# Optimization experiments

Hardware: AMD Instinct MI355X
Metric: run time of the kernel (lower is better)

Reference implementation:

```python
import jax, jax.numpy as jnp
import numpy as np

N_NODES = 65536   # 64 graphs * 1024 nodes
N_EDGES = 1048576
B, S = 64, 1024   # graphs, nodes per graph (regular batching)
C_IN, H = 4, 128


def _p(key, shape, scale=0.05):
    return scale * jax.random.normal(key, shape, dtype=jnp.float32)


def setup_inputs() -> dict:
    ks = jax.random.split(jax.random.key(0), 32)
    x = jax.random.normal(ks[0], (N_NODES, C_IN), dtype=jnp.float32)
    # edges drawn uniformly over nodes (PyG [2, E] convention)
    edge_index = jax.random.randint(ks[1], (2, N_EDGES), 0, N_NODES)
    batch = jnp.repeat(jnp.arange(B), S)  # contiguous, equal-size graphs
    inp = {"x": x, "edge_index": edge_index, "batch": batch}
    # GCN layers
    inp["gW1"] = _p(ks[2], (C_IN, H)); inp["gb1"] = jnp.zeros((H,), jnp.float32)
    inp["gW2"] = _p(ks[3], (H, H));    inp["gb2"] = jnp.zeros((H,), jnp.float32)
    # Residual block 1 (C_IN -> H, 1x1 conv shortcut). BN in eval mode with
    # running_mean=0, running_var=1 folds to gamma*x + beta.
    inp["r1w1"] = _p(ks[4], (H, C_IN, 3)); inp["r1b1"] = jnp.zeros((H,), jnp.float32)
    inp["r1g1"] = jnp.ones((H,), jnp.float32); inp["r1be1"] = jnp.zeros((H,), jnp.float32)
    inp["r1w2"] = _p(ks[5], (H, H, 3)); inp["r1b2"] = jnp.zeros((H,), jnp.float32)
    inp["r1g2"] = jnp.ones((H,), jnp.float32); inp["r1be2"] = jnp.zeros((H,), jnp.float32)
    inp["r1sw"] = _p(ks[6], (H, C_IN, 1)); inp["r1sb"] = jnp.zeros((H,), jnp.float32)
    # Residual block 2 (H -> H, identity shortcut)
    inp["r2w1"] = _p(ks[7], (H, H, 3)); inp["r2b1"] = jnp.zeros((H,), jnp.float32)
    inp["r2g1"] = jnp.ones((H,), jnp.float32); inp["r2be1"] = jnp.zeros((H,), jnp.float32)
    inp["r2w2"] = _p(ks[8], (H, H, 3)); inp["r2b2"] = jnp.zeros((H,), jnp.float32)
    inp["r2g2"] = jnp.ones((H,), jnp.float32); inp["r2be2"] = jnp.zeros((H,), jnp.float32)
    return inp


def _gcn(h, W, b, row, col, dinv_row, dinv_col, n):
    # PyG GCNConv: h' = D^-1/2 (A + I) D^-1/2 (h W) + b
    hw = h @ W                                   # [n, out]
    norm = dinv_row * dinv_col                   # [E+n]
    msg = norm[:, None] * hw[row]                # gather src
    return jax.ops.segment_sum(msg, col, num_segments=n) + b


def _conv1d(x, w, b, pad):
    y = jax.lax.conv_general_dilated(x, w, (1,), [(pad, pad)],
                                     dimension_numbers=("NCH", "OIH", "NCH"))
    return y + b[None, :, None]


def _resblock(x, w1, b1, g1, be1, w2, b2, g2, be2, sw=None, sb=None):
    y = _conv1d(x, w1, b1, 1)
    y = jax.nn.relu(g1[None, :, None] * y + be1[None, :, None])
    y = _conv1d(y, w2, b2, 1)
    y = g2[None, :, None] * y + be2[None, :, None]
    sc = x if sw is None else _conv1d(x, sw, sb, 0)
    return jax.nn.relu(y + sc)


def reference(x, edge_index, batch, gW1, gb1, gW2, gb2,
              r1w1, r1b1, r1g1, r1be1, r1w2, r1b2, r1g2, r1be2, r1sw, r1sb,
              r2w1, r2b1, r2g1, r2be1, r2w2, r2b2, r2g2, r2be2):
    n = x.shape[0]
    loop = jnp.arange(n)
    row = jnp.concatenate([edge_index[0], loop])   # src (+ self loops)
    col = jnp.concatenate([edge_index[1], loop])   # dst (+ self loops)
    deg = jax.ops.segment_sum(jnp.ones_like(col, dtype=x.dtype), col, num_segments=n)
    dinv = jnp.where(deg > 0, jax.lax.rsqrt(deg), 0.0)
    dinv_row, dinv_col = dinv[row], dinv[col]

    h = jax.nn.relu(_gcn(x, gW1, gb1, row, col, dinv_row, dinv_col, n))
    h = jax.nn.relu(_gcn(h, gW2, gb2, row, col, dinv_row, dinv_col, n))

    # to_dense_batch: batch is contiguous with S nodes per graph -> reshape,
    # then transpose to [B, C, S] for Conv1d.
    xd = x.reshape(B, S, C_IN).transpose(0, 2, 1)
    f = _resblock(xd, r1w1, r1b1, r1g1, r1be1, r1w2, r1b2, r1g2, r1be2, r1sw, r1sb)
    f = _resblock(f, r2w1, r2b1, r2g1, r2be1, r2w2, r2b2, r2g2, r2be2)
    global_reps = f.mean(axis=2)                   # [B, H]
    return h, global_reps
```

## Files before the change

### kernel.cpp

```cpp
#include <hip/hip_runtime.h>
#include <hip/hip_bf16.h>
#include <cstddef>
#include <cstdint>

#define NN 65536
#define NE 1048576
#define BGR 64
#define SGR 1024
#define HH 128
#define BCAP 5120
#define SSTRIDE 64

typedef unsigned short ushort_t;
typedef __attribute__((ext_vector_type(8))) short short8v;
typedef __attribute__((ext_vector_type(4))) float f32x4;

static __device__ inline ushort_t f2bf(float f) {
    __hip_bfloat16 h = __float2bfloat16(f);
    return *reinterpret_cast<ushort_t*>(&h);
}
static __device__ inline float bflo(unsigned int u) { return __uint_as_float(u << 16); }
static __device__ inline float bfhi(unsigned int u) { return __uint_as_float(u & 0xffff0000u); }


__global__ void prep_k(const float* __restrict__ r1w1, const float* __restrict__ r1w2,
                       const float* __restrict__ r2w1, const float* __restrict__ r2w2,
                       const float* __restrict__ gW2,
                       float* __restrict__ wT1, ushort_t* __restrict__ wbB,
                       ushort_t* __restrict__ wbC, ushort_t* __restrict__ wbD,
                       ushort_t* __restrict__ w2T, ushort_t* __restrict__ zA,
                       ushort_t* __restrict__ f1, float* __restrict__ gout,
                       int* __restrict__ bucketFill) {
    int gid = blockIdx.x * 256 + threadIdx.x;
    if (gid < 1536) {
        int o = gid & 127, k = (gid >> 7) % 3, ci = gid / 384;
        wT1[ci * 384 + k * 128 + o] = r1w1[o * 12 + ci * 3 + k];
    } else if (gid < 1536 + 3 * 49152) {
        int idx = gid - 1536;
        int which = idx / 49152; idx -= which * 49152;
        int ci = idx & 127, o = (idx >> 7) & 127, k = idx >> 14;
        const float* w = which == 0 ? r1w2 : (which == 1 ? r2w1 : r2w2);
        ushort_t* wb = which == 0 ? wbB : (which == 1 ? wbC : wbD);
        wb[idx] = f2bf(w[o * 384 + ci * 3 + k]);
    } else if (gid < 1536 + 3 * 49152 + 16384) {
        int idx = gid - (1536 + 3 * 49152);
        int k = idx & 127, h = idx >> 7;
        w2T[idx] = f2bf(gW2[k * 128 + h]);
    } else if (gid < 1536 + 3 * 49152 + 16384 + 16384) {
        int idx = gid - (1536 + 3 * 49152 + 16384);
        int b = idx >> 8, r = (idx >> 7) & 1, c = idx & 127;
        size_t off = ((size_t)b * 1026 + (r ? 1025 : 0)) * 128 + c;
        zA[off] = 0;
        f1[off] = 0;
    } else if (gid < 1536 + 3 * 49152 + 16384 + 16384 + 8192) {
        gout[gid - (1536 + 3 * 49152 + 16384 + 16384)] = 0.f;
    } else if (gid < 1536 + 3 * 49152 + 16384 + 16384 + 8192 + 256) {
        bucketFill[gid - (1536 + 3 * 49152 + 16384 + 16384 + 8192)] = 0;
    }
}


static __device__ __forceinline__ void binA_body(int blk,
        const int* __restrict__ row, const int* __restrict__ col,
        int* __restrict__ bucketFill, unsigned* __restrict__ region) {
    __shared__ int lcnt[256], lbase[256], lcur[256];
    int t = threadIdx.x;
    lcnt[t] = 0;
    __syncthreads();
    int e0 = blk * 4096;
    int r[16], c[16];
    #pragma unroll
    for (int i = 0; i < 16; ++i) {
        int e = e0 + i * 256 + t;
        r[i] = row[e];
        c[i] = col[e];
        atomicAdd(&lcnt[(unsigned)c[i] >> 8], 1);
    }
    __syncthreads();
    lbase[t] = atomicAdd(&bucketFill[t], lcnt[t]);
    lcur[t] = 0;
    __syncthreads();
    #pragma unroll
    for (int i = 0; i < 16; ++i) {
        int bkt = (unsigned)c[i] >> 8;
        int pos = lbase[bkt] + atomicAdd(&lcur[bkt], 1);
        if (pos < BCAP)
            region[bkt * BCAP + pos] = ((unsigned)r[i] << 8) | ((unsigned)c[i] & 255u);
    }
}

static __device__ __forceinline__ void binB_body(int blk,
        const unsigned* __restrict__ region, const int* __restrict__ bucketFill,
        unsigned* __restrict__ slots4, int* __restrict__ cnts, float* __restrict__ dinv) {
    __shared__ int deg[256], cur[256];
    int t = threadIdx.x, b = blk;
    deg[t] = 0;
    __syncthreads();
    int cnt = min(bucketFill[b], BCAP);
    const unsigned* reg = region + b * BCAP;
    for (int i = t; i < cnt; i += 256)
        atomicAdd(&deg[reg[i] & 255u], 1);
    __syncthreads();
    int dg = deg[t];
    int n = (b << 8) + t;
    cnts[n] = dg;
    dinv[n] = rsqrtf((float)(dg + 1));
    cur[t] = 0;
    __syncthreads();
    for (int i = t; i < cnt; i += 256) {
        unsigned en = reg[i];
        int d8 = en & 255u;
        int rk = atomicAdd(&cur[d8], 1);
        if (rk < 63)
            slots4[((size_t)((b << 8) + d8)) * SSTRIDE + rk] = en >> 8;
    }
    __syncthreads();
    int L = min(dg, 63);
    size_t base = (size_t)n * SSTRIDE;
    slots4[base + L] = (unsigned)n;
    int E8 = (L + 8) & ~7;
    for (int j = L + 1; j < E8; ++j) slots4[base + j] = 0xFFFFFFFFu;
}


static __device__ __forceinline__ void aggx_body(int blk,
        const float* __restrict__ x, const int* __restrict__ cnts,
        const float* __restrict__ dinv, unsigned* __restrict__ slots4,
        const float* __restrict__ W1, const float* __restrict__ b1,
        ushort_t* __restrict__ h1out) {
    int w = threadIdx.x >> 6, lane = threadIdx.x & 63;
    int n = blk * 4 + w;
    int L = min(cnts[n], 63);
    int E8 = (L + 8) & ~7;
    float dn = dinv[n];
    size_t base = (size_t)n * SSTRIDE;
    unsigned src = (unsigned)n;
    float wgt = 0.f;
    if (lane < E8) {
        unsigned e = slots4[base + lane];
        if (e != 0xFFFFFFFFu) { src = e; wgt = dn * dinv[e]; }
        slots4[base + lane] = ((unsigned)f2bf(wgt) << 16) | src;
    }
    float4 xv = *(const float4*)&x[(size_t)src * 4];
    float a0 = wgt * xv.x, a1 = wgt * xv.y, a2 = wgt * xv.z, a3 = wgt * xv.w;
    #pragma unroll
    for (int d = 1; d < 64; d <<= 1) {
        a0 += __shfl_xor(a0, d);
        a1 += __shfl_xor(a1, d);
        a2 += __shfl_xor(a2, d);
        a3 += __shfl_xor(a3, d);
    }
    int c2 = lane * 2;
    float s0 = b1[c2]     + a0 * W1[c2]     + a1 * W1[128 + c2] + a2 * W1[256 + c2] + a3 * W1[384 + c2];
    float s1 = b1[c2 + 1] + a0 * W1[c2 + 1] + a1 * W1[129 + c2] + a2 * W1[257 + c2] + a3 * W1[385 + c2];
    s0 = fmaxf(s0, 0.f);
    s1 = fmaxf(s1, 0.f);
    unsigned p = (unsigned)f2bf(s0) | ((unsigned)f2bf(s1) << 16);
    *(unsigned*)&h1out[(size_t)n * 128 + c2] = p;
}

__global__ __launch_bounds__(256) void agg2y_k(const ushort_t* __restrict__ h1,
                                               const int* __restrict__ cnts,
                                               const unsigned* __restrict__ slots4,
                                               ushort_t* __restrict__ Y) {
    int w = threadIdx.x >> 6, lane = threadIdx.x & 63;
    int q = lane >> 4, l = lane & 15;
    int n = blockIdx.x * 16 + w * 4 + q;
    int c8 = l * 8;
    int L = min(cnts[n], 63);
    int iters = ((L + 8) & ~7) >> 3;
    const unsigned* sl4 = slots4 + (size_t)n * SSTRIDE;
    float a0 = 0, a1 = 0, a2 = 0, a3 = 0, a4 = 0, a5 = 0, a6 = 0, a7 = 0;
#define ACC8(v, ww) do { \
        a0 = fmaf(ww, bflo((v).x), a0); a1 = fmaf(ww, bfhi((v).x), a1); \
        a2 = fmaf(ww, bflo((v).y), a2); a3 = fmaf(ww, bfhi((v).y), a3); \
        a4 = fmaf(ww, bflo((v).z), a4); a5 = fmaf(ww, bfhi((v).z), a5); \
        a6 = fmaf(ww, bflo((v).w), a6); a7 = fmaf(ww, bfhi((v).w), a7); } while (0)
    for (int i = 0; i < iters; ++i) {
        uint4 e0 = *(const uint4*)&sl4[i * 8];
        uint4 e1 = *(const uint4*)&sl4[i * 8 + 4];
        uint4 v0 = *(const uint4*)&h1[(size_t)(e0.x & 0xffffu) * 128 + c8];
        uint4 v1 = *(const uint4*)&h1[(size_t)(e0.y & 0xffffu) * 128 + c8];
        uint4 v2 = *(const uint4*)&h1[(size_t)(e0.z & 0xffffu) * 128 + c8];
        uint4 v3 = *(const uint4*)&h1[(size_t)(e0.w & 0xffffu) * 128 + c8];
        uint4 v4 = *(const uint4*)&h1[(size_t)(e1.x & 0xffffu) * 128 + c8];
        uint4 v5 = *(const uint4*)&h1[(size_t)(e1.y & 0xffffu) * 128 + c8];
        uint4 v6 = *(const uint4*)&h1[(size_t)(e1.z & 0xffffu) * 128 + c8];
        uint4 v7 = *(const uint4*)&h1[(size_t)(e1.w & 0xffffu) * 128 + c8];
        ACC8(v0, bfhi(e0.x));
        ACC8(v1, bfhi(e0.y));
        ACC8(v2, bfhi(e0.z));
        ACC8(v3, bfhi(e0.w));
        ACC8(v4, bfhi(e1.x));
        ACC8(v5, bfhi(e1.y));
        ACC8(v6, bfhi(e1.z));
        ACC8(v7, bfhi(e1.w));
    }
#undef ACC8
    uint4 p;
    p.x = (unsigned)f2bf(a0) | ((unsigned)f2bf(a1) << 16);
    p.y = (unsigned)f2bf(a2) | ((unsigned)f2bf(a3) << 16);
    p.z = (unsigned)f2bf(a4) | ((unsigned)f2bf(a5) << 16);
    p.w = (unsigned)f2bf(a6) | ((unsigned)f2bf(a7) << 16);
    *(uint4*)&Y[(size_t)n * 128 + c8] = p;
}

static __device__ __forceinline__ void gemm_body(int blk,
        const ushort_t* __restrict__ A, const ushort_t* __restrict__ Bt,
        const float* __restrict__ b2, float* __restrict__ out) {
    int t = threadIdx.x, w = t >> 6, lane = t & 63;
    int l15 = lane & 15, lk = lane >> 4;
    int n0 = blk * 128;
    int wr = w >> 1, wc = w & 1;
    f32x4 acc[4][4] = {};
    for (int kc = 0; kc < 128; kc += 32) {
        short8v a[4], bb[4];
        #pragma unroll
        for (int nf = 0; nf < 4; ++nf)
            a[nf] = *(const short8v*)&A[(size_t)(n0 + wr * 64 + nf * 16 + l15) * 128 + kc + lk * 8];
        #pragma unroll
        for (int hf = 0; hf < 4; ++hf)
            bb[hf] = *(const short8v*)&Bt[(size_t)(wc * 64 + hf * 16 + l15) * 128 + kc + lk * 8];
        #pragma unroll
        for (int nf = 0; nf < 4; ++nf)
            #pragma unroll
            for (int hf = 0; hf < 4; ++hf)
                acc[nf][hf] = __builtin_amdgcn_mfma_f32_16x16x32_bf16(a[nf], bb[hf], acc[nf][hf], 0, 0, 0);
    }
    #pragma unroll
    for (int nf = 0; nf < 4; ++nf)
        #pragma unroll
        for (int hf = 0; hf < 4; ++hf) {
            int col = wc * 64 + hf * 16 + l15;
            float bv = b2[col];
            #pragma unroll
            for (int r = 0; r < 4; ++r)
                out[(size_t)(n0 + wr * 64 + nf * 16 + lk * 4 + r) * 128 + col] =
                    fmaxf(acc[nf][hf][r] + bv, 0.f);
        }
}


static __device__ __forceinline__ void convA_body(int blk,
        const float* __restrict__ x, const float* __restrict__ wT,
        const float* __restrict__ b1, const float* __restrict__ g1, const float* __restrict__ be1,
        const float* __restrict__ sw, const float* __restrict__ sb,
        ushort_t* __restrict__ z1, ushort_t* __restrict__ sc) {
    __shared__ float wl[4 * 384];
    __shared__ float zl[4][66];
    int t = threadIdx.x;
    int b = blk >> 4, tile = blk & 15;
    int s0 = tile * 64;
    int og = t & 31, sg = t >> 5, o0 = og * 4;
    for (int idx = t; idx < 4 * 384; idx += 256) wl[idx] = wT[idx];
    for (int idx = t; idx < 4 * 66; idx += 256) {
        int cl = idx / 66, pos = idx % 66;
        int s = s0 - 1 + pos;
        zl[cl][pos] = (s >= 0 && s < SGR) ? x[((size_t)b * SGR + s) * 4 + cl] : 0.f;
    }
    __syncthreads();
    float acc[4][8] = {};
    float scv[4][8] = {};
    for (int cl = 0; cl < 4; ++cl) {
        float sws[4];
        #pragma unroll
        for (int oi = 0; oi < 4; ++oi) sws[oi] = sw[(o0 + oi) * 4 + cl];
        #pragma unroll
        for (int k = 0; k < 3; ++k) {
            const float4 wv = *(const float4*)&wl[cl * 384 + k * 128 + o0];
            float wvv[4] = {wv.x, wv.y, wv.z, wv.w};
            #pragma unroll
            for (int j = 0; j < 8; ++j) {
                float zv = zl[cl][sg * 8 + j + k];
                #pragma unroll
                for (int oi = 0; oi < 4; ++oi) acc[oi][j] += wvv[oi] * zv;
            }
        }
        #pragma unroll
        for (int j = 0; j < 8; ++j) {
            float zc = zl[cl][sg * 8 + j + 1];
            #pragma unroll
            for (int oi = 0; oi < 4; ++oi) scv[oi][j] += sws[oi] * zc;
        }
    }
    float gg[4], bbv[4], eev[4], sbv[4];
    #pragma unroll
    for (int oi = 0; oi < 4; ++oi) {
        int o = o0 + oi;
        gg[oi] = g1[o]; bbv[oi] = b1[o]; eev[oi] = be1[o]; sbv[oi] = sb[o];
    }
    #pragma unroll
    for (int j = 0; j < 8; ++j) {
        int s = s0 + sg * 8 + j;
        uint64_t pz = 0, ps = 0;
        #pragma unroll
        for (int oi = 0; oi < 4; ++oi) {
            float v = gg[oi] * (acc[oi][j] + bbv[oi]) + eev[oi];
            v = fmaxf(v, 0.f);
            pz |= (uint64_t)f2bf(v) << (16 * oi);
            ps |= (uint64_t)f2bf(scv[oi][j] + sbv[oi]) << (16 * oi);
        }
        *(uint64_t*)&z1[((size_t)b * 1026 + 1 + s) * 128 + o0] = pz;
        *(uint64_t*)&sc[((size_t)b * SGR + s) * 128 + o0] = ps;
    }
}

template <int MODE>
static __device__ __forceinline__ void conv_body(int cblk,
        const ushort_t* __restrict__ zin, const ushort_t* __restrict__ wb,
        const float* __restrict__ bias, const float* __restrict__ gam,
        const float* __restrict__ bet, const ushort_t* __restrict__ res,
        void* __restrict__ outp, ushort_t* __restrict__ zl) {
    int t = threadIdx.x;
    int b = cblk >> 3, s0 = (cblk & 7) << 7;
    const ushort_t* zg = zin + ((size_t)b * 1026 + s0) * 128;
    for (int idx = t; idx < 130 * 16; idx += 256) {
        int r = idx >> 4, c = idx & 15;
        *(short8v*)&zl[r * 128 + c * 8] = *(const short8v*)&zg[(size_t)r * 128 + ((c ^ (r & 7)) * 8)];
    }
    __syncthreads();
    int w = t >> 6, lane = t & 63;
    int wr = w >> 1, wc = w & 1;
    int l15 = lane & 15, lk = lane >> 4;
    f32x4 acc[4][4] = {};
    #pragma unroll
    for (int k = 0; k < 3; ++k) {
        const ushort_t* wk = wb + k * 16384;
        #pragma unroll
        for (int cc = 0; cc < 4; ++cc) {
            short8v a[4], bf[4];
            #pragma unroll
            for (int of = 0; of < 4; ++of)
                a[of] = *(const short8v*)&wk[(size_t)(wr * 64 + of * 16 + l15) * 128 + cc * 32 + lk * 8];
            #pragma unroll
            for (int sf = 0; sf < 4; ++sf) {
                int r = wc * 64 + sf * 16 + l15 + k;
                int chunk = (cc * 4 + lk) ^ (r & 7);
                bf[sf] = *(const short8v*)&zl[r * 128 + chunk * 8];
            }
            #pragma unroll
            for (int of = 0; of < 4; ++of)
                #pragma unroll
                for (int sf = 0; sf < 4; ++sf)
                    acc[of][sf] = __builtin_amdgcn_mfma_f32_16x16x32_bf16(a[of], bf[sf], acc[of][sf], 0, 0, 0);
        }
    }
    float psum[4][4];
    if (MODE == 2)
        #pragma unroll
        for (int of = 0; of < 4; ++of)
            #pragma unroll
            for (int r = 0; r < 4; ++r) psum[of][r] = 0.f;
    #pragma unroll
    for (int of = 0; of < 4; ++of) {
        int o_ = wr * 64 + of * 16 + lk * 4;
        float g4[4], b4[4], e4[4];
        *(float4*)g4 = *(const float4*)&gam[o_];
        *(float4*)b4 = *(const float4*)&bias[o_];
        *(float4*)e4 = *(const float4*)&bet[o_];
        #pragma unroll
        for (int sf = 0; sf < 4; ++sf) {
            int s_ = s0 + wc * 64 + sf * 16 + l15;
            float v[4];
            #pragma unroll
            for (int r = 0; r < 4; ++r) v[r] = g4[r] * (acc[of][sf][r] + b4[r]) + e4[r];
            if (MODE == 1) {
                uint2 rv = *(const uint2*)&res[((size_t)b * SGR + s_) * 128 + o_];
                v[0] += bflo(rv.x); v[1] += bfhi(rv.x);
                v[2] += bflo(rv.y); v[3] += bfhi(rv.y);
            }
            if (MODE == 2) {
                uint2 rv = *(const uint2*)&res[((size_t)b * 1026 + 1 + s_) * 128 + o_];
                v[0] += bflo(rv.x); v[1] += bfhi(rv.x);
                v[2] += bflo(rv.y); v[3] += bfhi(rv.y);
            }
            #pragma unroll
            for (int r = 0; r < 4; ++r) v[r] = fmaxf(v[r], 0.f);
            if (MODE <= 1) {
                uint64_t p = (uint64_t)f2bf(v[0]) | ((uint64_t)f2bf(v[1]) << 16) |
                             ((uint64_t)f2bf(v[2]) << 32) | ((uint64_t)f2bf(v[3]) << 48);
                *(uint64_t*)&((ushort_t*)outp)[((size_t)b * 1026 + 1 + s_) * 128 + o_] = p;
            } else {
                #pragma unroll
                for (int r = 0; r < 4; ++r) psum[of][r] += v[r];
            }
        }
    }
    if (MODE == 2) {
        float* gout = (float*)outp;
        #pragma unroll
        for (int of = 0; of < 4; ++of) {
            #pragma unroll
            for (int r = 0; r < 4; ++r) {
                float t2 = psum[of][r];
                t2 += __shfl_xor(t2, 1);
                t2 += __shfl_xor(t2, 2);
                t2 += __shfl_xor(t2, 4);
                t2 += __shfl_xor(t2, 8);
                if (l15 == 0)
                    atomicAdd(&gout[b * 128 + wr * 64 + of * 16 + lk * 4 + r], t2 * (1.0f / 1024.0f));
            }
        }
    }
}


__global__ __launch_bounds__(256) void k2_binA_convA(
        const int* __restrict__ row, const int* __restrict__ col,
        int* __restrict__ bucketFill, unsigned* __restrict__ region,
        const float* __restrict__ x, const float* __restrict__ wT1,
        const float* __restrict__ b1, const float* __restrict__ g1,
        const float* __restrict__ be1, const float* __restrict__ sw,
        const float* __restrict__ sb, ushort_t* __restrict__ zA,
        ushort_t* __restrict__ scb) {
    if (blockIdx.x < 256)
        binA_body(blockIdx.x, row, col, bucketFill, region);
    else
        convA_body(blockIdx.x - 256, x, wT1, b1, g1, be1, sw, sb, zA, scb);
}

__global__ __launch_bounds__(256) void k3_binB_convB(
        const unsigned* __restrict__ region, const int* __restrict__ bucketFill,
        unsigned* __restrict__ slots4, int* __restrict__ cnts, float* __restrict__ dinv,
        const ushort_t* __restrict__ zA, const ushort_t* __restrict__ wbB,
        const float* __restrict__ b2, const float* __restrict__ g2,
        const float* __restrict__ be2, const ushort_t* __restrict__ scb,
        ushort_t* __restrict__ f1) {
    __shared__ ushort_t zl[130 * 128];
    if (blockIdx.x < 256)
        binB_body(blockIdx.x, region, bucketFill, slots4, cnts, dinv);
    else
        conv_body<1>(blockIdx.x - 256, zA, wbB, b2, g2, be2, scb, f1, zl);
}

__global__ __launch_bounds__(256) void k4_aggx_convC(
        const float* __restrict__ x, const int* __restrict__ cnts,
        const float* __restrict__ dinv, unsigned* __restrict__ slots4,
        const float* __restrict__ W1, const float* __restrict__ b1g,
        ushort_t* __restrict__ h1out,
        const ushort_t* __restrict__ f1, const ushort_t* __restrict__ wbC,
        const float* __restrict__ b3, const float* __restrict__ g3,
        const float* __restrict__ be3, ushort_t* __restrict__ zA) {
    __shared__ ushort_t zl[130 * 128];
    if (blockIdx.x < 16384)
        aggx_body(blockIdx.x, x, cnts, dinv, slots4, W1, b1g, h1out);
    else
        conv_body<0>(blockIdx.x - 16384, f1, wbC, b3, g3, be3, nullptr, zA, zl);
}

__global__ __launch_bounds__(256) void k6_gemm_convD(
        const ushort_t* __restrict__ Y, const ushort_t* __restrict__ w2T,
        const float* __restrict__ gb2, float* __restrict__ hout,
        const ushort_t* __restrict__ zA, const ushort_t* __restrict__ wbD,
        const float* __restrict__ b4, const float* __restrict__ g4,
        const float* __restrict__ be4, const ushort_t* __restrict__ f1,
        float* __restrict__ gout) {
    __shared__ ushort_t zl[130 * 128];
    if (blockIdx.x < 512)
        gemm_body(blockIdx.x, Y, w2T, gb2, hout);
    else
        conv_body<2>(blockIdx.x - 512, zA, wbD, b4, g4, be4, f1, gout, zl);
}


extern "C" void kernel_launch(void* const* d_in, const int* in_sizes, int n_in,
                              void* d_out, int out_size, void* d_ws, size_t ws_size,
                              hipStream_t stream) {
    const float* x    = (const float*)d_in[0];
    const int*   ei   = (const int*)d_in[1];
    const float* gW1  = (const float*)d_in[3];
    const float* gb1  = (const float*)d_in[4];
    const float* gW2  = (const float*)d_in[5];
    const float* gb2  = (const float*)d_in[6];
    const float* r1w1 = (const float*)d_in[7];
    const float* r1b1 = (const float*)d_in[8];
    const float* r1g1 = (const float*)d_in[9];
    const float* r1be1= (const float*)d_in[10];
    const float* r1w2 = (const float*)d_in[11];
    const float* r1b2 = (const float*)d_in[12];
    const float* r1g2 = (const float*)d_in[13];
    const float* r1be2= (const float*)d_in[14];
    const float* r1sw = (const float*)d_in[15];
    const float* r1sb = (const float*)d_in[16];
    const float* r2w1 = (const float*)d_in[17];
    const float* r2b1 = (const float*)d_in[18];
    const float* r2g1 = (const float*)d_in[19];
    const float* r2be1= (const float*)d_in[20];
    const float* r2w2 = (const float*)d_in[21];
    const float* r2b2 = (const float*)d_in[22];
    const float* r2g2 = (const float*)d_in[23];
    const float* r2be2= (const float*)d_in[24];

    float* hout = (float*)d_out;
    float* gout = (float*)d_out + (size_t)NN * HH;

    ushort_t* bufT = (ushort_t*)d_ws;
    ushort_t* zA   = bufT + (size_t)NN * 128;
    ushort_t* f1   = zA + (size_t)64 * 1026 * 128;
    ushort_t* scb  = f1 + (size_t)64 * 1026 * 128;
    unsigned* slots4 = (unsigned*)(scb + (size_t)64 * 1024 * 128);
    ushort_t* wbB  = (ushort_t*)(slots4 + (size_t)NN * SSTRIDE);
    ushort_t* wbC  = wbB + 49152;
    ushort_t* wbD  = wbC + 49152;
    ushort_t* w2T  = wbD + 49152;
    float* wT1     = (float*)(w2T + 16384);
    float* dinv    = wT1 + 1536;
    int* cnts      = (int*)(dinv + NN);
    int* bucketFill= cnts + NN;
    unsigned* region = (unsigned*)bufT;

    const int* row = ei;
    const int* col = ei + NE;
    ushort_t* h1buf = scb;

    prep_k<<<743, 256, 0, stream>>>(r1w1, r1w2, r2w1, r2w2, gW2,
                                    wT1, wbB, wbC, wbD, w2T, zA, f1, gout, bucketFill);
    k2_binA_convA<<<256 + BGR * 16, 256, 0, stream>>>(
        row, col, bucketFill, region,
        x, wT1, r1b1, r1g1, r1be1, r1sw, r1sb, zA, scb);
    k3_binB_convB<<<256 + BGR * 8, 256, 0, stream>>>(
        region, bucketFill, slots4, cnts, dinv,
        zA, wbB, r1b2, r1g2, r1be2, scb, f1);
    k4_aggx_convC<<<NN / 4 + BGR * 8, 256, 0, stream>>>(
        x, cnts, dinv, slots4, gW1, gb1, h1buf,
        f1, wbC, r2b1, r2g1, r2be1, zA);
    agg2y_k<<<NN / 16, 256, 0, stream>>>(h1buf, cnts, slots4, bufT);
    k6_gemm_convD<<<512 + BGR * 8, 256, 0, stream>>>(
        bufT, w2T, gb2, hout,
        zA, wbD, r2b2, r2g2, r2be2, f1, gout);
}
```

Measured before the change: 202.9 us.

## Halve conv tile size and interleave heterogeneous block roles in fused kernels

Conv blocks now cover 64 positions instead of 128, which doubles the conv block count and shrinks LDS use from 130 to 66 rows. In every fused kernel, block IDs are interleaved so graph-work blocks (binning, aggregation, GEMM) and conv blocks are spread evenly across the grid instead of sitting in two contiguous ranges. The aim is better occupancy and load balance across CUs so the two kinds of work overlap. In exchange, weight reuse per block drops, since each weight fragment now feeds 2 MFMAs instead of 4, so there is more weight traffic from global memory or cache.

Result: slower. 235.1 us (+15.9%).

```diff
diff --git a/kernel.cpp b/kernel.cpp
--- a/kernel.cpp
+++ b/kernel.cpp
@@ -312,9 +312,9 @@
         const float* __restrict__ bet, const ushort_t* __restrict__ res,
         void* __restrict__ outp, ushort_t* __restrict__ zl) {
     int t = threadIdx.x;
-    int b = cblk >> 3, s0 = (cblk & 7) << 7;
+    int b = cblk >> 4, s0 = (cblk & 15) << 6;
     const ushort_t* zg = zin + ((size_t)b * 1026 + s0) * 128;
-    for (int idx = t; idx < 130 * 16; idx += 256) {
+    for (int idx = t; idx < 66 * 16; idx += 256) {
         int r = idx >> 4, c = idx & 15;
         *(short8v*)&zl[r * 128 + c * 8] = *(const short8v*)&zg[(size_t)r * 128 + ((c ^ (r & 7)) * 8)];
     }
@@ -322,26 +322,26 @@
     int w = t >> 6, lane = t & 63;
     int wr = w >> 1, wc = w & 1;
     int l15 = lane & 15, lk = lane >> 4;
-    f32x4 acc[4][4] = {};
+    f32x4 acc[4][2] = {};
     #pragma unroll
     for (int k = 0; k < 3; ++k) {
         const ushort_t* wk = wb + k * 16384;
         #pragma unroll
         for (int cc = 0; cc < 4; ++cc) {
-            short8v a[4], bf[4];
+            short8v a[4], bf[2];
             #pragma unroll
             for (int of = 0; of < 4; ++of)
                 a[of] = *(const short8v*)&wk[(size_t)(wr * 64 + of * 16 + l15) * 128 + cc * 32 + lk * 8];
             #pragma unroll
-            for (int sf = 0; sf < 4; ++sf) {
-                int r = wc * 64 + sf * 16 + l15 + k;
+            for (int sf = 0; sf < 2; ++sf) {
+                int r = wc * 32 + sf * 16 + l15 + k;
                 int chunk = (cc * 4 + lk) ^ (r & 7);
                 bf[sf] = *(const short8v*)&zl[r * 128 + chunk * 8];
             }
             #pragma unroll
             for (int of = 0; of < 4; ++of)
                 #pragma unroll
-                for (int sf = 0; sf < 4; ++sf)
+                for (int sf = 0; sf < 2; ++sf)
                     acc[of][sf] = __builtin_amdgcn_mfma_f32_16x16x32_bf16(a[of], bf[sf], acc[of][sf], 0, 0, 0);
         }
     }
@@ -359,8 +359,8 @@
         *(float4*)b4 = *(const float4*)&bias[o_];
         *(float4*)e4 = *(const float4*)&bet[o_];
         #pragma unroll
-        for (int sf = 0; sf < 4; ++sf) {
-            int s_ = s0 + wc * 64 + sf * 16 + l15;
+        for (int sf = 0; sf < 2; ++sf) {
+            int s_ = s0 + wc * 32 + sf * 16 + l15;
             float v[4];
             #pragma unroll
             for (int r = 0; r < 4; ++r) v[r] = g4[r] * (acc[of][sf][r] + b4[r]) + e4[r];
@@ -413,10 +413,11 @@
         const float* __restrict__ be1, const float* __restrict__ sw,
         const float* __restrict__ sb, ushort_t* __restrict__ zA,
         ushort_t* __restrict__ scb) {
-    if (blockIdx.x < 256)
-        binA_body(blockIdx.x, row, col, bucketFill, region);
+    int q = blockIdx.x / 5, r = blockIdx.x % 5;
+    if (r == 4)
+        binA_body(q, row, col, bucketFill, region);
     else
-        convA_body(blockIdx.x - 256, x, wT1, b1, g1, be1, sw, sb, zA, scb);
+        convA_body(q * 4 + r, x, wT1, b1, g1, be1, sw, sb, zA, scb);
 }
 
 __global__ __launch_bounds__(256) void k3_binB_convB(
@@ -426,11 +427,12 @@
         const float* __restrict__ b2, const float* __restrict__ g2,
         const float* __restrict__ be2, const ushort_t* __restrict__ scb,
         ushort_t* __restrict__ f1) {
-    __shared__ ushort_t zl[130 * 128];
-    if (blockIdx.x < 256)
-        binB_body(blockIdx.x, region, bucketFill, slots4, cnts, dinv);
+    __shared__ ushort_t zl[66 * 128];
+    int q = blockIdx.x / 5, r = blockIdx.x % 5;
+    if (r == 4)
+        binB_body(q, region, bucketFill, slots4, cnts, dinv);
     else
-        conv_body<1>(blockIdx.x - 256, zA, wbB, b2, g2, be2, scb, f1, zl);
+        conv_body<1>(q * 4 + r, zA, wbB, b2, g2, be2, scb, f1, zl);
 }
 
 __global__ __launch_bounds__(256) void k4_aggx_convC(
@@ -441,11 +443,12 @@
         const ushort_t* __restrict__ f1, const ushort_t* __restrict__ wbC,
         const float* __restrict__ b3, const float* __restrict__ g3,
         const float* __restrict__ be3, ushort_t* __restrict__ zA) {
-    __shared__ ushort_t zl[130 * 128];
-    if (blockIdx.x < 16384)
-        aggx_body(blockIdx.x, x, cnts, dinv, slots4, W1, b1g, h1out);
+    __shared__ ushort_t zl[66 * 128];
+    int q = blockIdx.x / 17, r = blockIdx.x % 17;
+    if (r == 16)
+        conv_body<0>(q, f1, wbC, b3, g3, be3, nullptr, zA, zl);
     else
-        conv_body<0>(blockIdx.x - 16384, f1, wbC, b3, g3, be3, nullptr, zA, zl);
+        aggx_body(q * 16 + r, x, cnts, dinv, slots4, W1, b1g, h1out);
 }
 
 __global__ __launch_bounds__(256) void k6_gemm_convD(
@@ -455,11 +458,12 @@
         const float* __restrict__ b4, const float* __restrict__ g4,
         const float* __restrict__ be4, const ushort_t* __restrict__ f1,
         float* __restrict__ gout) {
-    __shared__ ushort_t zl[130 * 128];
-    if (blockIdx.x < 512)
-        gemm_body(blockIdx.x, Y, w2T, gb2, hout);
+    __shared__ ushort_t zl[66 * 128];
+    int q = blockIdx.x / 3, r = blockIdx.x % 3;
+    if (r == 0)
+        gemm_body(q, Y, w2T, gb2, hout);
     else
-        conv_body<2>(blockIdx.x - 512, zA, wbD, b4, g4, be4, f1, gout, zl);
+        conv_body<2>(q * 2 + (r - 1), zA, wbD, b4, g4, be4, f1, gout, zl);
 }
 
 
@@ -515,17 +519,17 @@
 
     prep_k<<<743, 256, 0, stream>>>(r1w1, r1w2, r2w1, r2w2, gW2,
                                     wT1, wbB, wbC, wbD, w2T, zA, f1, gout, bucketFill);
-    k2_binA_convA<<<256 + BGR * 16, 256, 0, stream>>>(
+    k2_binA_convA<<<1280, 256, 0, stream>>>(
         row, col, bucketFill, region,
         x, wT1, r1b1, r1g1, r1be1, r1sw, r1sb, zA, scb);
-    k3_binB_convB<<<256 + BGR * 8, 256, 0, stream>>>(
+    k3_binB_convB<<<1280, 256, 0, stream>>>(
         region, bucketFill, slots4, cnts, dinv,
         zA, wbB, r1b2, r1g2, r1be2, scb, f1);
-    k4_aggx_convC<<<NN / 4 + BGR * 8, 256, 0, stream>>>(
+    k4_aggx_convC<<<17408, 256, 0, stream>>>(
         x, cnts, dinv, slots4, gW1, gb1, h1buf,
         f1, wbC, r2b1, r2g1, r2be1, zA);
     agg2y_k<<<NN / 16, 256, 0, stream>>>(h1buf, cnts, slots4, bufT);
-    k6_gemm_convD<<<512 + BGR * 8, 256, 0, stream>>>(
+    k6_gemm_convD<<<1536, 256, 0, stream>>>(
         bufT, w2T, gb2, hout,
         zA, wbD, r2b2, r2g2, r2be2, f1, gout);
 }
```

## Aggregate 4-channel inputs first and recompute layer-1 features inside second aggregation

Applied to the files above, without the earlier changes.

The first GCN layer no longer writes a 128-wide bf16 h1 buffer. It stores only the 4-float aggregated inputs per node, and the second aggregation gathers those 16-byte rows and recomputes relu(y·W1+b1) on the fly. This swaps a 256-byte-per-edge gather for a 16-byte one at the cost of extra FMAs per edge. Slot padding changes from multiples of 8 to multiples of 4, and the fused aggx/convC kernel is split into two separate launches.

Measured after the change: 173.0 us, median of 2. 1.17x faster.

```diff
diff --git a/kernel.cpp b/kernel.cpp
--- a/kernel.cpp
+++ b/kernel.cpp
@@ -118,25 +118,25 @@
     int L = min(dg, 63);
     size_t base = (size_t)n * SSTRIDE;
     slots4[base + L] = (unsigned)n;
-    int E8 = (L + 8) & ~7;
-    for (int j = L + 1; j < E8; ++j) slots4[base + j] = 0xFFFFFFFFu;
-}
-
-
-static __device__ __forceinline__ void aggx_body(int blk,
-        const float* __restrict__ x, const int* __restrict__ cnts,
-        const float* __restrict__ dinv, unsigned* __restrict__ slots4,
-        const float* __restrict__ W1, const float* __restrict__ b1,
-        ushort_t* __restrict__ h1out) {
+    int E4 = (L + 4) & ~3;
+    for (int j = L + 1; j < E4; ++j) slots4[base + j] = 0xFFFFFFFFu;
+}
+
+
+__global__ __launch_bounds__(256) void aggy_k(const float* __restrict__ x,
+                                              const int* __restrict__ cnts,
+                                              const float* __restrict__ dinv,
+                                              unsigned* __restrict__ slots4,
+                                              float* __restrict__ y4) {
     int w = threadIdx.x >> 6, lane = threadIdx.x & 63;
-    int n = blk * 4 + w;
+    int n = blockIdx.x * 4 + w;
     int L = min(cnts[n], 63);
-    int E8 = (L + 8) & ~7;
+    int E4 = (L + 4) & ~3;
     float dn = dinv[n];
     size_t base = (size_t)n * SSTRIDE;
     unsigned src = (unsigned)n;
     float wgt = 0.f;
-    if (lane < E8) {
+    if (lane < E4) {
         unsigned e = slots4[base + lane];
         if (e != 0xFFFFFFFFu) { src = e; wgt = dn * dinv[e]; }
         slots4[base + lane] = ((unsigned)f2bf(wgt) << 16) | src;
@@ -150,58 +150,59 @@
         a2 += __shfl_xor(a2, d);
         a3 += __shfl_xor(a3, d);
     }
-    int c2 = lane * 2;
-    float s0 = b1[c2]     + a0 * W1[c2]     + a1 * W1[128 + c2] + a2 * W1[256 + c2] + a3 * W1[384 + c2];
-    float s1 = b1[c2 + 1] + a0 * W1[c2 + 1] + a1 * W1[129 + c2] + a2 * W1[257 + c2] + a3 * W1[385 + c2];
-    s0 = fmaxf(s0, 0.f);
-    s1 = fmaxf(s1, 0.f);
-    unsigned p = (unsigned)f2bf(s0) | ((unsigned)f2bf(s1) << 16);
-    *(unsigned*)&h1out[(size_t)n * 128 + c2] = p;
-}
-
-__global__ __launch_bounds__(256) void agg2y_k(const ushort_t* __restrict__ h1,
+    if (lane == 0) *(float4*)&y4[(size_t)n * 4] = make_float4(a0, a1, a2, a3);
+}
+
+__global__ __launch_bounds__(256) void agg2h_k(const float* __restrict__ y4,
                                                const int* __restrict__ cnts,
                                                const unsigned* __restrict__ slots4,
+                                               const float* __restrict__ W1,
+                                               const float* __restrict__ b1,
                                                ushort_t* __restrict__ Y) {
-    int w = threadIdx.x >> 6, lane = threadIdx.x & 63;
+    int t = threadIdx.x, w = t >> 6, lane = t & 63;
     int q = lane >> 4, l = lane & 15;
     int n = blockIdx.x * 16 + w * 4 + q;
     int c8 = l * 8;
+    float w1r[4][8], b1r[8];
+    #pragma unroll
+    for (int k = 0; k < 4; ++k) {
+        *(float4*)&w1r[k][0] = *(const float4*)&W1[k * 128 + c8];
+        *(float4*)&w1r[k][4] = *(const float4*)&W1[k * 128 + c8 + 4];
+    }
+    *(float4*)&b1r[0] = *(const float4*)&b1[c8];
+    *(float4*)&b1r[4] = *(const float4*)&b1[c8 + 4];
     int L = min(cnts[n], 63);
-    int iters = ((L + 8) & ~7) >> 3;
+    int iters = ((L + 4) & ~3) >> 2;
     const unsigned* sl4 = slots4 + (size_t)n * SSTRIDE;
-    float a0 = 0, a1 = 0, a2 = 0, a3 = 0, a4 = 0, a5 = 0, a6 = 0, a7 = 0;
-#define ACC8(v, ww) do { \
-        a0 = fmaf(ww, bflo((v).x), a0); a1 = fmaf(ww, bfhi((v).x), a1); \
-        a2 = fmaf(ww, bflo((v).y), a2); a3 = fmaf(ww, bfhi((v).y), a3); \
-        a4 = fmaf(ww, bflo((v).z), a4); a5 = fmaf(ww, bfhi((v).z), a5); \
-        a6 = fmaf(ww, bflo((v).w), a6); a7 = fmaf(ww, bfhi((v).w), a7); } while (0)
+    float a[8] = {0, 0, 0, 0, 0, 0, 0, 0};
+#define ACCH(yv, ww) do { \
+        _Pragma("unroll") \
+        for (int j = 0; j < 8; ++j) { \
+            float h = b1r[j]; \
+            h = fmaf((yv).x, w1r[0][j], h); \
+            h = fmaf((yv).y, w1r[1][j], h); \
+            h = fmaf((yv).z, w1r[2][j], h); \
+            h = fmaf((yv).w, w1r[3][j], h); \
+            h = fmaxf(h, 0.f); \
+            a[j] = fmaf(ww, h, a[j]); \
+        } } while (0)
     for (int i = 0; i < iters; ++i) {
-        uint4 e0 = *(const uint4*)&sl4[i * 8];
-        uint4 e1 = *(const uint4*)&sl4[i * 8 + 4];
-        uint4 v0 = *(const uint4*)&h1[(size_t)(e0.x & 0xffffu) * 128 + c8];
-        uint4 v1 = *(const uint4*)&h1[(size_t)(e0.y & 0xffffu) * 128 + c8];
-        uint4 v2 = *(const uint4*)&h1[(size_t)(e0.z & 0xffffu) * 128 + c8];
-        uint4 v3 = *(const uint4*)&h1[(size_t)(e0.w & 0xffffu) * 128 + c8];
-        uint4 v4 = *(const uint4*)&h1[(size_t)(e1.x & 0xffffu) * 128 + c8];
-        uint4 v5 = *(const uint4*)&h1[(size_t)(e1.y & 0xffffu) * 128 + c8];
-        uint4 v6 = *(const uint4*)&h1[(size_t)(e1.z & 0xffffu) * 128 + c8];
-        uint4 v7 = *(const uint4*)&h1[(size_t)(e1.w & 0xffffu) * 128 + c8];
-        ACC8(v0, bfhi(e0.x));
-        ACC8(v1, bfhi(e0.y));
-        ACC8(v2, bfhi(e0.z));
-        ACC8(v3, bfhi(e0.w));
-        ACC8(v4, bfhi(e1.x));
-        ACC8(v5, bfhi(e1.y));
-        ACC8(v6, bfhi(e1.z));
-        ACC8(v7, bfhi(e1.w));
-    }
-#undef ACC8
+        uint4 e = *(const uint4*)&sl4[i * 4];
+        float4 y0 = *(const float4*)&y4[(size_t)(e.x & 0xffffu) * 4];
+        float4 y1 = *(const float4*)&y4[(size_t)(e.y & 0xffffu) * 4];
+        float4 y2 = *(const float4*)&y4[(size_t)(e.z & 0xffffu) * 4];
+        float4 y3 = *(const float4*)&y4[(size_t)(e.w & 0xffffu) * 4];
+        ACCH(y0, bfhi(e.x));
+        ACCH(y1, bfhi(e.y));
+        ACCH(y2, bfhi(e.z));
+        ACCH(y3, bfhi(e.w));
+    }
+#undef ACCH
     uint4 p;
-    p.x = (unsigned)f2bf(a0) | ((unsigned)f2bf(a1) << 16);
-    p.y = (unsigned)f2bf(a2) | ((unsigned)f2bf(a3) << 16);
-    p.z = (unsigned)f2bf(a4) | ((unsigned)f2bf(a5) << 16);
-    p.w = (unsigned)f2bf(a6) | ((unsigned)f2bf(a7) << 16);
+    p.x = (unsigned)f2bf(a[0]) | ((unsigned)f2bf(a[1]) << 16);
+    p.y = (unsigned)f2bf(a[2]) | ((unsigned)f2bf(a[3]) << 16);
+    p.z = (unsigned)f2bf(a[4]) | ((unsigned)f2bf(a[5]) << 16);
+    p.w = (unsigned)f2bf(a[6]) | ((unsigned)f2bf(a[7]) << 16);
     *(uint4*)&Y[(size_t)n * 128 + c8] = p;
 }
 
@@ -433,22 +434,15 @@
         conv_body<1>(blockIdx.x - 256, zA, wbB, b2, g2, be2, scb, f1, zl);
 }
 
-__global__ __launch_bounds__(256) void k4_aggx_convC(
-        const float* __restrict__ x, const int* __restrict__ cnts,
-        const float* __restrict__ dinv, unsigned* __restrict__ slots4,
-        const float* __restrict__ W1, const float* __restrict__ b1g,
-        ushort_t* __restrict__ h1out,
+__global__ __launch_bounds__(256) void convC_k(
         const ushort_t* __restrict__ f1, const ushort_t* __restrict__ wbC,
         const float* __restrict__ b3, const float* __restrict__ g3,
         const float* __restrict__ be3, ushort_t* __restrict__ zA) {
     __shared__ ushort_t zl[130 * 128];
-    if (blockIdx.x < 16384)
-        aggx_body(blockIdx.x, x, cnts, dinv, slots4, W1, b1g, h1out);
-    else
-        conv_body<0>(blockIdx.x - 16384, f1, wbC, b3, g3, be3, nullptr, zA, zl);
-}
-
-__global__ __launch_bounds__(256) void k6_gemm_convD(
+    conv_body<0>(blockIdx.x, f1, wbC, b3, g3, be3, nullptr, zA, zl);
+}
+
+__global__ __launch_bounds__(256) void k7_gemm_convD(
         const ushort_t* __restrict__ Y, const ushort_t* __restrict__ w2T,
         const float* __restrict__ gb2, float* __restrict__ hout,
         const ushort_t* __restrict__ zA, const ushort_t* __restrict__ wbD,
@@ -507,11 +501,11 @@
     float* dinv    = wT1 + 1536;
     int* cnts      = (int*)(dinv + NN);
     int* bucketFill= cnts + NN;
+    float* ybuf    = (float*)(bucketFill + 256);
     unsigned* region = (unsigned*)bufT;
 
     const int* row = ei;
     const int* col = ei + NE;
-    ushort_t* h1buf = scb;
 
     prep_k<<<743, 256, 0, stream>>>(r1w1, r1w2, r2w1, r2w2, gW2,
                                     wT1, wbB, wbC, wbD, w2T, zA, f1, gout, bucketFill);
@@ -521,11 +515,10 @@
     k3_binB_convB<<<256 + BGR * 8, 256, 0, stream>>>(
         region, bucketFill, slots4, cnts, dinv,
         zA, wbB, r1b2, r1g2, r1be2, scb, f1);
-    k4_aggx_convC<<<NN / 4 + BGR * 8, 256, 0, stream>>>(
-        x, cnts, dinv, slots4, gW1, gb1, h1buf,
-        f1, wbC, r2b1, r2g1, r2be1, zA);
-    agg2y_k<<<NN / 16, 256, 0, stream>>>(h1buf, cnts, slots4, bufT);
-    k6_gemm_convD<<<512 + BGR * 8, 256, 0, stream>>>(
+    aggy_k<<<NN / 4, 256, 0, stream>>>(x, cnts, dinv, slots4, ybuf);
+    convC_k<<<BGR * 8, 256, 0, stream>>>(f1, wbC, r2b1, r2g1, r2be1, zA);
+    agg2h_k<<<NN / 16, 256, 0, stream>>>(ybuf, cnts, slots4, gW1, gb1, bufT);
+    k7_gemm_convD<<<1024, 256, 0, stream>>>(
         bufT, w2T, gb2, hout,
         zA, wbD, r2b2, r2g2, r2be2, f1, gout);
 }
```
